# Performance work log

Measured on AMD Instinct MI355X. Metric: run time of the kernel, lower is better.

Reference implementation:

```python
import jax, jax.numpy as jnp
import numpy as np

D = 1024      # d_model
H = 16        # num_heads
HW = D // H   # head_width = 64
FF = 4 * D    # hidden_dim = 4096
BATCH = 2
T = 2048
EPS = 1e-5


def layer_norm(x, g, b):
    mu = jnp.mean(x, axis=-1, keepdims=True)
    var = jnp.mean(jnp.square(x - mu), axis=-1, keepdims=True)
    return (x - mu) * jax.lax.rsqrt(var + EPS) * g + b


def setup_inputs() -> dict:
    key = jax.random.key(0)
    ks = jax.random.split(key, 7)
    s = 0.02
    return {
        "x": jax.random.normal(ks[0], (BATCH, T, D), dtype=jnp.float32),
        "Wq": jax.random.normal(ks[1], (D, D), dtype=jnp.float32) * s,
        "Wk": jax.random.normal(ks[2], (D, D), dtype=jnp.float32) * s,
        "Wv": jax.random.normal(ks[3], (D, D), dtype=jnp.float32) * s,
        "W1": jax.random.normal(ks[4], (FF, D), dtype=jnp.float32) * s,
        "W2": jax.random.normal(ks[5], (D, FF), dtype=jnp.float32) * s,
        "g1": jnp.ones((D,), dtype=jnp.float32),
        "b1": jnp.zeros((D,), dtype=jnp.float32),
        "g2": jnp.ones((D,), dtype=jnp.float32),
        "b2": jnp.zeros((D,), dtype=jnp.float32),
    }


def reference(x, Wq, Wk, Wv, W1, W2, g1, b1, g2, b2):
    N, t, d = x.shape
    # norm1
    xn = layer_norm(x, g1, b1)

    # --- MHSA with ALiBi + causal mask (math mirrors torch module) ---
    def heads(y):  # (N,t,D) -> (N,H,t,HW)
        return y.reshape(N, t, H, HW).transpose(0, 2, 1, 3)

    q = heads(xn @ Wq.T)
    k = heads(xn @ Wk.T)
    v = heads(xn @ Wv.T)

    scores = jnp.einsum("nhqd,nhkd->nhqk", q, k) / np.sqrt(HW).astype(np.float32)

    pos = jnp.arange(t)
    rel = (pos[None, :] - pos[:, None]).astype(x.dtype)           # [t,t], rel[i,j]=j-i
    slopes = (2.0 ** (-(jnp.arange(1, H + 1)) * (8.0 / H))).astype(x.dtype)  # [H]
    alibi = slopes[:, None, None] * rel                            # [H,t,t]
    causal = jnp.where(pos[None, :] > pos[:, None],
                       jnp.array(-jnp.inf, x.dtype),
                       jnp.array(0.0, x.dtype))                    # [t,t]

    att = jax.nn.softmax(scores + alibi[None] + causal[None, None], axis=-1)
    o = jnp.einsum("nhqk,nhkd->nhqd", att, v)
    o = o.transpose(0, 2, 1, 3).reshape(N, t, d)

    att_out = xn + o

    # --- MLP: Linear -> SiLU -> Linear ---
    h = layer_norm(att_out, g2, b2)
    m = jax.nn.silu(h @ W1.T) @ W2.T
    return att_out + m
```

## Files before the change

### kernel.cpp

```cpp
#include <hip/hip_runtime.h>

#define DMODEL 1024
#define NHEAD  16
#define HWID   64
#define FFDIM  4096
#define NBATCH 2
#define SEQT   2048
#define NTOK   4096
#define QKLD   3072

using bf8    = __attribute__((ext_vector_type(8))) short;
using f32x4  = __attribute__((ext_vector_type(4))) float;
using f32x16 = __attribute__((ext_vector_type(16))) float;

__device__ inline short to_bf16(float f) {
  unsigned u = __float_as_uint(f);
  return (short)((u + 0x7fffu + ((u >> 16) & 1u)) >> 16);
}
__device__ inline float from_bf16(short s) {
  return __uint_as_float(((unsigned)(unsigned short)s) << 16);
}
__device__ inline float exp2_fast(float x) {
  float r;
  asm("v_exp_f32 %0, %1" : "=v"(r) : "v"(x));
  return r;
}
__device__ inline unsigned cvt_pk_bf16(float lo, float hi) {
  unsigned r;
  asm("v_cvt_pk_bf16_f32 %0, %1, %2" : "=v"(r) : "v"(lo), "v"(hi));
  return r;
}
__device__ inline void lds_load16(const void* g, void* l) {
  __builtin_amdgcn_global_load_lds(
      (const __attribute__((address_space(1))) void*)g,
      (__attribute__((address_space(3))) void*)l, 16, 0, 0);
}

__global__ __launch_bounds__(256)
void cvt_all(const float* __restrict__ Wq, const float* __restrict__ Wk,
             const float* __restrict__ Wv, const float* __restrict__ W1,
             const float* __restrict__ W2, short* __restrict__ wqkv,
             short* __restrict__ w1b, short* __restrict__ w2b) {
  int i = blockIdx.x * 256 + threadIdx.x;
  const float* src;
  short* dst;
  if (i < 1048576)      { src = W1; dst = w1b; }
  else if (i < 2097152) { src = W2; dst = w2b;            i -= 1048576; }
  else if (i < 2359296) { src = Wq; dst = wqkv;           i -= 2097152; }
  else if (i < 2621440) { src = Wk; dst = wqkv + 1048576; i -= 2359296; }
  else                  { src = Wv; dst = wqkv + 2097152; i -= 2621440; }
  float4 v = ((const float4*)src)[i];
  short4 o;
  o.x = to_bf16(v.x); o.y = to_bf16(v.y);
  o.z = to_bf16(v.z); o.w = to_bf16(v.w);
  ((short4*)dst)[i] = o;
}

__global__ __launch_bounds__(256)
void ln_kernel(const float* __restrict__ x, const float* __restrict__ g,
               const float* __restrict__ b, short* __restrict__ out) {
  const int row = blockIdx.x;
  const int t = threadIdx.x;
  const float4 v = ((const float4*)(x + (long)row * DMODEL))[t];
  float s  = v.x + v.y + v.z + v.w;
  float s2 = v.x * v.x + v.y * v.y + v.z * v.z + v.w * v.w;
#pragma unroll
  for (int m = 1; m < 64; m <<= 1) {
    s  += __shfl_xor(s, m);
    s2 += __shfl_xor(s2, m);
  }
  __shared__ float red[8];
  if ((t & 63) == 0) { red[t >> 6] = s; red[4 + (t >> 6)] = s2; }
  __syncthreads();
  s  = red[0] + red[1] + red[2] + red[3];
  s2 = red[4] + red[5] + red[6] + red[7];
  const float mu = s * (1.f / DMODEL);
  const float rs = rsqrtf(s2 * (1.f / DMODEL) - mu * mu + 1e-5f);
  const float4 gv = ((const float4*)g)[t];
  const float4 bv = ((const float4*)b)[t];
  short4 o;
  o.x = to_bf16((v.x - mu) * rs * gv.x + bv.x);
  o.y = to_bf16((v.y - mu) * rs * gv.y + bv.y);
  o.z = to_bf16((v.z - mu) * rs * gv.z + bv.z);
  o.w = to_bf16((v.w - mu) * rs * gv.w + bv.w);
  ((short4*)(out + (long)row * DMODEL))[t] = o;
}

template <int EPI>
__global__ __launch_bounds__(512, 2)
void gemm8r(const short* __restrict__ A, const short* __restrict__ Bw,
            void* __restrict__ Cout, int N, int lda, int ldb, int Kslice,
            long zstride) {
  __shared__ short lds[4][16384];
  const int tid = threadIdx.x;
  const int wid = tid >> 6, lane = tid & 63;
  const int l15 = lane & 15, l4 = lane >> 4;
  const int wm = wid >> 2, wn = wid & 3;

  const int gx = gridDim.x, nwg = gx * gridDim.y;
  const int wg = blockIdx.y * gx + blockIdx.x;
  const int sw = (wg & 7) * (nwg >> 3) + (wg >> 3);
  const int sx = gx >> 2;
  const int st = sw >> 4, w16 = sw & 15;
  const long bm = (long)((st / sx) * 4 + (w16 >> 2)) * 256;
  const long bn = (long)((st % sx) * 4 + (w16 & 3)) * 256;
  const long kofs = (long)blockIdx.z * Kslice;

  long aoff[2], boff[2];
  int  doff[2];
#pragma unroll
  for (int l = 0; l < 2; ++l) {
    const int gid = l * 512 + tid;
    const int row = gid >> 2;
    const int sg = (gid & 3) ^ ((row >> 1) & 3);
    aoff[l] = (bm + row) * (long)lda + kofs + sg * 8;
    boff[l] = (bn + row) * (long)ldb + kofs + sg * 8;
    doff[l] = gid * 16;
  }
  int offA[8], offB[4];
#pragma unroll
  for (int m = 0; m < 8; ++m) {
    const int row = wm * 128 + m * 16 + l15;
    offA[m] = row * 64 + ((l4 ^ ((row >> 1) & 3)) << 4);
  }
#pragma unroll
  for (int n = 0; n < 4; ++n) {
    const int row = wn * 64 + n * 16 + l15;
    offB[n] = row * 64 + ((l4 ^ ((row >> 1) & 3)) << 4);
  }

  const int NT = Kslice >> 5;
  f32x4 acc[8][4] = {};
  bf8 fa0[8], fb0[4], fa1[8], fb1[4];

#pragma unroll
  for (int tt = 0; tt < 3; ++tt) {
    char* db = (char*)&lds[tt][0];
#pragma unroll
    for (int l = 0; l < 2; ++l) {
      lds_load16(A  + aoff[l] + tt * 32, db + doff[l]);
      lds_load16(Bw + boff[l] + tt * 32, db + 16384 + doff[l]);
    }
  }
  asm volatile("s_waitcnt vmcnt(8)" ::: "memory");
  __builtin_amdgcn_s_barrier();
  asm volatile("" ::: "memory");
  {
    const char* sb = (const char*)&lds[0][0];
#pragma unroll
    for (int m = 0; m < 8; ++m) fa0[m] = *(const bf8*)(sb + offA[m]);
#pragma unroll
    for (int n = 0; n < 4; ++n) fb0[n] = *(const bf8*)(sb + 16384 + offB[n]);
  }

  auto step = [&](int t, bf8 (&ca)[8], bf8 (&cb)[4],
                  bf8 (&na)[8], bf8 (&nb)[4]) {
    if (t + 3 < NT) asm volatile("s_waitcnt vmcnt(4)" ::: "memory");
    else            asm volatile("s_waitcnt vmcnt(0)" ::: "memory");
    __builtin_amdgcn_s_barrier();
    asm volatile("" ::: "memory");
    if (t + 3 < NT) {
      char* db = (char*)&lds[(t + 3) & 3][0];
      const long ks = (long)(t + 3) * 32;
#pragma unroll
      for (int l = 0; l < 2; ++l) {
        lds_load16(A  + aoff[l] + ks, db + doff[l]);
        lds_load16(Bw + boff[l] + ks, db + 16384 + doff[l]);
      }
    }
    if (t + 1 < NT) {
      const char* sb = (const char*)&lds[(t + 1) & 3][0];
#pragma unroll
      for (int m = 0; m < 8; ++m) na[m] = *(const bf8*)(sb + offA[m]);
#pragma unroll
      for (int n = 0; n < 4; ++n) nb[n] = *(const bf8*)(sb + 16384 + offB[n]);
    }
    __builtin_amdgcn_sched_barrier(0);
    __builtin_amdgcn_s_setprio(1);
#pragma unroll
    for (int m = 0; m < 8; ++m)
#pragma unroll
      for (int n = 0; n < 4; ++n)
        acc[m][n] = __builtin_amdgcn_mfma_f32_16x16x32_bf16(ca[m], cb[n], acc[m][n], 0, 0, 0);
    __builtin_amdgcn_s_setprio(0);
  };

  for (int t = 0; t < NT; t += 2) {
    step(t,     fa0, fb0, fa1, fb1);
    step(t + 1, fa1, fb1, fa0, fb0);
  }

  float* Cp = (float*)Cout + (EPI == 2 ? (long)blockIdx.z * zstride : 0);
#pragma unroll
  for (int m = 0; m < 8; ++m)
#pragma unroll
    for (int n = 0; n < 4; ++n) {
      const long col = bn + wn * 64 + n * 16 + l15;
#pragma unroll
      for (int r = 0; r < 4; ++r) {
        const long row = bm + wm * 128 + m * 16 + l4 * 4 + r;
        float v = acc[m][n][r];
        if (EPI == 0) {
          ((short*)Cout)[row * N + col] = to_bf16(v);
        } else if (EPI == 1) {
          ((short*)Cout)[row * N + col] = to_bf16(v / (1.f + __expf(-v)));
        } else {
          Cp[row * N + col] = v;
        }
      }
    }
}

__global__ __launch_bounds__(256)
void pack_kv(const short* __restrict__ qkv, short* __restrict__ Kp,
             short* __restrict__ Vp) {
  __shared__ short tile[64][72];
  const int bx = blockIdx.x, bh = blockIdx.y;
  const int b = bh >> 4, h = bh & 15;
  const int t = threadIdx.x;
  if (bx < 64) {
    const int g = bx;
    const int row = t >> 3, cc = t & 7, c = cc >> 1, hi = cc & 1;
    const bf8 v = *(const bf8*)&qkv[(long)(b * SEQT + g * 32 + row) * QKLD +
                                    1024 + h * HWID + c * 16 + hi * 8];
    *(bf8*)&Kp[(((long)bh * 256 + g * 4 + c) * 64 + hi * 32 + row) * 8] = v;
  } else {
    const int tc = bx - 64;
    {
      const int r = t >> 2, c = (t & 3) * 16;
      const long src = (long)(b * SEQT + tc * 64 + r) * QKLD + 2048 + h * HWID + c;
      *(bf8*)&tile[r][c]     = *(const bf8*)&qkv[src];
      *(bf8*)&tile[r][c + 8] = *(const bf8*)&qkv[src + 8];
    }
    __syncthreads();
    const int dg = t >> 7, ch = (t >> 5) & 3, row = t & 31;
#pragma unroll
    for (int hi = 0; hi < 2; ++hi) {
      short o[8];
#pragma unroll
      for (int j = 0; j < 8; ++j) o[j] = tile[ch * 16 + hi * 8 + j][dg * 32 + row];
      *(bf8*)&Vp[(((long)bh * 256 + dg * 128 + tc * 4 + ch) * 64 + hi * 32 + row) * 8] =
          *(bf8*)o;
    }
  }
}

__global__ __launch_bounds__(64, 2)
void attn_kernel(const short* __restrict__ qkv, const short* __restrict__ Kp,
                 const short* __restrict__ Vp, const short* __restrict__ xn,
                 float* __restrict__ att) {
  const int L = blockIdx.x;
  const int bh = (L & 7) * 4 + ((L >> 3) & 3);
  const int qtile = 63 - (L >> 5);
  const int b = bh >> 4, h = bh & 15;
  const int q0 = qtile * 32;
  const int lane = threadIdx.x;
  const int l31 = lane & 31, hi = lane >> 5;
  const long tokbase = (long)b * SEQT;

  bf8 qf[4];
  {
    const short* qrow = qkv + (tokbase + q0 + l31) * QKLD + h * HWID + hi * 8;
#pragma unroll
    for (int c = 0; c < 4; ++c) qf[c] = *(const bf8*)(qrow + c * 16);
  }

  const float slope2 = exp2f(-0.5f * (float)(h + 1)) * 1.44269504f;
  const float sc2 = 0.125f * 1.44269504f;
  float arr[16];
#pragma unroll
  for (int r = 0; r < 16; ++r) arr[r] = slope2 * (float)((r & 3) + 8 * (r >> 2));
  const float hofs = slope2 * 4.f * (float)hi;
  const float qabs = (float)(q0 + l31);

  float m2 = -1e30f, lsum = 0.f;
  f32x16 acc0 = {}, acc1 = {};
  const int ktm = q0 >> 6;
  const bf8* kfb = (const bf8*)Kp + (long)bh * 16384 + lane;
  const bf8* vfb = (const bf8*)Vp + (long)bh * 16384 + lane;

  bf8 kc[8], kn[8], vc[8];
#pragma unroll
  for (int c = 0; c < 4; ++c) {
    kc[c]     = kfb[c * 64];
    kc[4 + c] = kfb[256 + c * 64];
  }

#pragma unroll 2
  for (int kt = 0; kt <= ktm; ++kt) {
    const int k0 = kt * 64;
    const long vb = (long)kt * 256;
#pragma unroll
    for (int ch = 0; ch < 4; ++ch) {
      vc[ch]     = vfb[vb + ch * 64];
      vc[4 + ch] = vfb[8192 + vb + ch * 64];
    }
    const long nb = (long)(kt < ktm ? kt + 1 : kt) * 512;
#pragma unroll
    for (int c = 0; c < 4; ++c) {
      kn[c]     = kfb[nb + c * 64];
      kn[4 + c] = kfb[nb + 256 + c * 64];
    }
    f32x16 s0 = {}, s1 = {};
#pragma unroll
    for (int c = 0; c < 4; ++c) {
      s0 = __builtin_amdgcn_mfma_f32_32x32x16_bf16(kc[c], qf[c], s0, 0, 0, 0);
      s1 = __builtin_amdgcn_mfma_f32_32x32x16_bf16(kc[4 + c], qf[c], s1, 0, 0, 0);
    }
    const float base = slope2 * ((float)k0 - qabs) + hofs;
    float s[32];
#pragma unroll
    for (int r = 0; r < 16; ++r) {
      s[r]      = fmaf(s0[r], sc2, base + arr[r]);
      s[16 + r] = fmaf(s1[r], sc2, base + arr[r] + slope2 * 32.f);
    }
    if (kt == ktm) {
      const int qi = q0 + l31;
#pragma unroll
      for (int r = 0; r < 16; ++r) {
        const int krel = (r & 3) + 8 * (r >> 2) + 4 * hi;
        if (k0 + krel > qi)      s[r]      = -1e30f;
        if (k0 + 32 + krel > qi) s[16 + r] = -1e30f;
      }
    }
    float ma = s[0], mb = s[1], mc = s[2], md = s[3];
#pragma unroll
    for (int i = 4; i < 32; i += 4) {
      ma = fmaxf(ma, s[i]); mb = fmaxf(mb, s[i + 1]);
      mc = fmaxf(mc, s[i + 2]); md = fmaxf(md, s[i + 3]);
    }
    float pm = fmaxf(fmaxf(ma, mb), fmaxf(mc, md));
    pm = fmaxf(pm, __shfl_xor(pm, 32));
    if (!__all(pm - m2 <= 11.0f)) {
      const float nm = fmaxf(m2, pm);
      const float alpha = exp2_fast(m2 - nm);
      m2 = nm;
      lsum *= alpha;
      acc0 *= alpha;
      acc1 *= alpha;
    }
    float p[32];
#pragma unroll
    for (int i = 0; i < 32; ++i) p[i] = exp2_fast(s[i] - m2);
    float sa = p[0], sb = p[1], sc = p[2], sd = p[3];
#pragma unroll
    for (int i = 4; i < 32; i += 4) {
      sa += p[i]; sb += p[i + 1]; sc += p[i + 2]; sd += p[i + 3];
    }
    float rs = (sa + sb) + (sc + sd);
    rs += __shfl_xor(rs, 32);
    lsum += rs;
    unsigned cpk[16];
#pragma unroll
    for (int g = 0; g < 8; ++g) {
      cpk[g]     = cvt_pk_bf16(p[2 * g], p[2 * g + 1]);
      cpk[8 + g] = cvt_pk_bf16(p[16 + 2 * g], p[16 + 2 * g + 1]);
    }
    bf8 pb[4];
#pragma unroll
    for (int ch = 0; ch < 4; ++ch) {
      const int cb = (ch >> 1) * 8 + (ch & 1) * 4;
      unsigned u0 = cpk[cb + 0], u2 = cpk[cb + 2];
      unsigned u1 = cpk[cb + 1], u3 = cpk[cb + 3];
      asm("v_permlane32_swap_b32 %0, %1" : "+v"(u0), "+v"(u2));
      asm("v_permlane32_swap_b32 %0, %1" : "+v"(u1), "+v"(u3));
      union { unsigned u[4]; bf8 v; } f;
      f.u[0] = u0; f.u[1] = u1; f.u[2] = u2; f.u[3] = u3;
      pb[ch] = f.v;
    }
#pragma unroll
    for (int ch = 0; ch < 4; ++ch) {
      acc0 = __builtin_amdgcn_mfma_f32_32x32x16_bf16(vc[ch], pb[ch], acc0, 0, 0, 0);
      acc1 = __builtin_amdgcn_mfma_f32_32x32x16_bf16(vc[4 + ch], pb[ch], acc1, 0, 0, 0);
    }
#pragma unroll
    for (int i = 0; i < 8; ++i) kc[i] = kn[i];
  }

  __shared__ float Os[32 * 68];
  const float rl = 1.f / lsum;
#pragma unroll
  for (int r = 0; r < 16; ++r) {
    const int d0 = (r & 3) + 8 * (r >> 2) + 4 * hi;
    Os[l31 * 68 + d0]      = acc0[r] * rl;
    Os[l31 * 68 + 32 + d0] = acc1[r] * rl;
  }
  __syncthreads();
#pragma unroll
  for (int it = 0; it < 8; ++it) {
    const int idx = it * 64 + lane;
    const int row = idx >> 4, c4 = idx & 15;
    const float4 ov = *(const float4*)&Os[row * 68 + c4 * 4];
    const long gbase = (tokbase + q0 + row) * DMODEL + h * HWID + c4 * 4;
    const short4 xv = *(const short4*)&xn[gbase];
    float4 o;
    o.x = ov.x + from_bf16(xv.x);
    o.y = ov.y + from_bf16(xv.y);
    o.z = ov.z + from_bf16(xv.z);
    o.w = ov.w + from_bf16(xv.w);
    *(float4*)&att[gbase] = o;
  }
}

__global__ __launch_bounds__(256)
void combine_kernel(const float* __restrict__ p, float* __restrict__ dout, int n4) {
  int i = blockIdx.x * 256 + threadIdx.x;
  if (i < n4) {
    float4 a  = ((const float4*)dout)[i];
    float4 b0 = ((const float4*)(p))[i];
    float4 b1 = ((const float4*)(p + 4194304))[i];
    float4 b2 = ((const float4*)(p + 8388608))[i];
    float4 b3 = ((const float4*)(p + 12582912))[i];
    a.x += (b0.x + b1.x) + (b2.x + b3.x);
    a.y += (b0.y + b1.y) + (b2.y + b3.y);
    a.z += (b0.z + b1.z) + (b2.z + b3.z);
    a.w += (b0.w + b1.w) + (b2.w + b3.w);
    ((float4*)dout)[i] = a;
  }
}

extern "C" void kernel_launch(void* const* d_in, const int* in_sizes, int n_in,
                              void* d_out, int out_size, void* d_ws, size_t ws_size,
                              hipStream_t stream) {
  (void)in_sizes; (void)n_in; (void)out_size; (void)ws_size;
  const float* x  = (const float*)d_in[0];
  const float* Wq = (const float*)d_in[1];
  const float* Wk = (const float*)d_in[2];
  const float* Wv = (const float*)d_in[3];
  const float* W1 = (const float*)d_in[4];
  const float* W2 = (const float*)d_in[5];
  const float* g1 = (const float*)d_in[6];
  const float* b1 = (const float*)d_in[7];
  const float* g2 = (const float*)d_in[8];
  const float* b2 = (const float*)d_in[9];

  char* ws = (char*)d_ws;
  const size_t MB = 1024 * 1024;
  short* wqkv_b = (short*)(ws + 0);
  short* w1_b   = (short*)(ws + 6  * MB);
  short* w2_b   = (short*)(ws + 14 * MB);
  short* xn     = (short*)(ws + 22 * MB);
  short* qkv    = (short*)(ws + 30 * MB);
  short* m1     = (short*)(ws + 22 * MB);
  short* Kp     = (short*)(ws + 54 * MB);
  short* Vp     = (short*)(ws + 62 * MB);
  short* hb     = (short*)(ws + 70 * MB);
  float* parts  = (float*)(ws + 54 * MB);
  float* att    = (float*)d_out;

  cvt_all<<<11264, 256, 0, stream>>>(Wq, Wk, Wv, W1, W2, wqkv_b, w1_b, w2_b);

  ln_kernel<<<NTOK, 256, 0, stream>>>(x, g1, b1, xn);

  gemm8r<0><<<dim3(12, 16), 512, 0, stream>>>(xn, wqkv_b, qkv, QKLD, DMODEL, DMODEL,
                                              DMODEL, 0);
  pack_kv<<<dim3(96, 32), 256, 0, stream>>>(qkv, Kp, Vp);

  attn_kernel<<<2048, 64, 0, stream>>>(qkv, Kp, Vp, xn, att);

  ln_kernel<<<NTOK, 256, 0, stream>>>(att, g2, b2, hb);

  gemm8r<1><<<dim3(16, 16), 512, 0, stream>>>(hb, w1_b, m1, FFDIM, DMODEL, DMODEL,
                                              DMODEL, 0);
  gemm8r<2><<<dim3(4, 16, 4), 512, 0, stream>>>(m1, w2_b, parts, DMODEL, FFDIM, FFDIM,
                                                1024, (long)NTOK * DMODEL);
  combine_kernel<<<4096, 256, 0, stream>>>(parts, (float*)d_out, 1048576);
}
```

Measured before the change: 204.8 us.

## Restructure GEMM into 64-wide K tiles with half-staged double-buffered LDS phases

New measurement: 209.0 us. 1.02x slower.

```diff
diff --git a/kernel.cpp b/kernel.cpp
--- a/kernel.cpp
+++ b/kernel.cpp
@@ -88,10 +88,10 @@
 
 template <int EPI>
 __global__ __launch_bounds__(512, 2)
-void gemm8r(const short* __restrict__ A, const short* __restrict__ Bw,
-            void* __restrict__ Cout, int N, int lda, int ldb, int Kslice,
-            long zstride) {
-  __shared__ short lds[4][16384];
+void gemm256(const short* __restrict__ A, const short* __restrict__ Bw,
+             void* __restrict__ Cout, int N, int lda, int ldb, int Kslice,
+             long zstride) {
+  __shared__ short lds[2][2][16384];
   const int tid = threadIdx.x;
   const int wid = tid >> 6, lane = tid & 63;
   const int l15 = lane & 15, l4 = lane >> 4;
@@ -105,101 +105,119 @@
   const long bm = (long)((st / sx) * 4 + (w16 >> 2)) * 256;
   const long bn = (long)((st % sx) * 4 + (w16 & 3)) * 256;
   const long kofs = (long)blockIdx.z * Kslice;
-
-  long aoff[2], boff[2];
-  int  doff[2];
+  const int NT = Kslice >> 6;
+
+  long arow[2], brow[2];
+  int  sgel[2], dofs[2];
 #pragma unroll
   for (int l = 0; l < 2; ++l) {
-    const int gid = l * 512 + tid;
-    const int row = gid >> 2;
-    const int sg = (gid & 3) ^ ((row >> 1) & 3);
-    aoff[l] = (bm + row) * (long)lda + kofs + sg * 8;
-    boff[l] = (bn + row) * (long)ldb + kofs + sg * 8;
-    doff[l] = gid * 16;
-  }
-  int offA[8], offB[4];
-#pragma unroll
-  for (int m = 0; m < 8; ++m) {
-    const int row = wm * 128 + m * 16 + l15;
-    offA[m] = row * 64 + ((l4 ^ ((row >> 1) & 3)) << 4);
-  }
-#pragma unroll
-  for (int n = 0; n < 4; ++n) {
-    const int row = wn * 64 + n * 16 + l15;
-    offB[n] = row * 64 + ((l4 ^ ((row >> 1) & 3)) << 4);
-  }
-
-  const int NT = Kslice >> 5;
+    const int g = l * 512 + tid;
+    const int row = g >> 2;
+    sgel[l] = ((g & 3) ^ (row & 3)) * 8;
+    dofs[l] = g * 16;
+    arow[l] = (bm + row) * (long)lda + kofs;
+    brow[l] = (bn + row) * (long)ldb + kofs;
+  }
+  auto stage_half = [&](int h) {
+    if (h >= (NT << 2)) return;
+    const int th = h >> 2, hi = h & 3, buf = th & 1;
+    const int ks = hi >> 1, isA = hi & 1;
+    char* db = (char*)&lds[buf][isA ? 0 : 1][0] + ks * 16384;
+    const long kb = (long)th * 64 + ks * 32;
+#pragma unroll
+    for (int l = 0; l < 2; ++l) {
+      const short* src = (isA ? A + arow[l] : Bw + brow[l]) + kb + sgel[l];
+      lds_load16(src, db + dofs[l]);
+    }
+  };
+
+  const int xsw = (l4 ^ (l15 & 3)) << 4;
+  const int aofs = (wm * 128 + l15) * 64 + xsw;
+  const int bofs = (wn * 64 + l15) * 64 + xsw;
+
   f32x4 acc[8][4] = {};
-  bf8 fa0[8], fb0[4], fa1[8], fb1[4];
-
-#pragma unroll
-  for (int tt = 0; tt < 3; ++tt) {
-    char* db = (char*)&lds[tt][0];
-#pragma unroll
-    for (int l = 0; l < 2; ++l) {
-      lds_load16(A  + aoff[l] + tt * 32, db + doff[l]);
-      lds_load16(Bw + boff[l] + tt * 32, db + 16384 + doff[l]);
-    }
-  }
-  asm volatile("s_waitcnt vmcnt(8)" ::: "memory");
+  bf8 fa[4], fa2[4], fb[4];
+
+#define PH_MID                                             \
+  __builtin_amdgcn_s_barrier();                            \
+  asm volatile("s_waitcnt lgkmcnt(0)" ::: "memory");       \
+  __builtin_amdgcn_sched_barrier(0);                       \
+  __builtin_amdgcn_s_setprio(1);
+#define PH_END                                             \
+  __builtin_amdgcn_s_setprio(0);                           \
+  __builtin_amdgcn_s_barrier();                            \
+  asm volatile("" ::: "memory");
+
+#pragma unroll
+  for (int h = 0; h < 7; ++h) stage_half(h);
+  asm volatile("s_waitcnt vmcnt(6)" ::: "memory");
   __builtin_amdgcn_s_barrier();
   asm volatile("" ::: "memory");
-  {
-    const char* sb = (const char*)&lds[0][0];
-#pragma unroll
-    for (int m = 0; m < 8; ++m) fa0[m] = *(const bf8*)(sb + offA[m]);
-#pragma unroll
-    for (int n = 0; n < 4; ++n) fb0[n] = *(const bf8*)(sb + 16384 + offB[n]);
-  }
-
-  auto step = [&](int t, bf8 (&ca)[8], bf8 (&cb)[4],
-                  bf8 (&na)[8], bf8 (&nb)[4]) {
-    if (t + 3 < NT) asm volatile("s_waitcnt vmcnt(4)" ::: "memory");
-    else            asm volatile("s_waitcnt vmcnt(0)" ::: "memory");
-    __builtin_amdgcn_s_barrier();
-    asm volatile("" ::: "memory");
-    if (t + 3 < NT) {
-      char* db = (char*)&lds[(t + 3) & 3][0];
-      const long ks = (long)(t + 3) * 32;
-#pragma unroll
-      for (int l = 0; l < 2; ++l) {
-        lds_load16(A  + aoff[l] + ks, db + doff[l]);
-        lds_load16(Bw + boff[l] + ks, db + 16384 + doff[l]);
-      }
-    }
-    if (t + 1 < NT) {
-      const char* sb = (const char*)&lds[(t + 1) & 3][0];
-#pragma unroll
-      for (int m = 0; m < 8; ++m) na[m] = *(const bf8*)(sb + offA[m]);
-#pragma unroll
-      for (int n = 0; n < 4; ++n) nb[n] = *(const bf8*)(sb + 16384 + offB[n]);
-    }
-    __builtin_amdgcn_sched_barrier(0);
-    __builtin_amdgcn_s_setprio(1);
-#pragma unroll
-    for (int m = 0; m < 8; ++m)
+
+  for (int u = 0; u < NT; ++u) {
+    const int buf = u & 1;
+    const char* pa = (const char*)&lds[buf][0][0];
+    const char* pb = (const char*)&lds[buf][1][0];
+#pragma unroll
+    for (int m = 0; m < 4; ++m) fa[m] = *(const bf8*)(pa + aofs + m * 1024);
+#pragma unroll
+    for (int n = 0; n < 4; ++n) fb[n] = *(const bf8*)(pb + bofs + n * 1024);
+    stage_half(4 * u + 7);
+    PH_MID
+#pragma unroll
+    for (int m = 0; m < 4; ++m)
 #pragma unroll
       for (int n = 0; n < 4; ++n)
-        acc[m][n] = __builtin_amdgcn_mfma_f32_16x16x32_bf16(ca[m], cb[n], acc[m][n], 0, 0, 0);
-    __builtin_amdgcn_s_setprio(0);
-  };
-
-  for (int t = 0; t < NT; t += 2) {
-    step(t,     fa0, fb0, fa1, fb1);
-    step(t + 1, fa1, fb1, fa0, fb0);
-  }
+        acc[m][n] = __builtin_amdgcn_mfma_f32_16x16x32_bf16(fa[m], fb[n], acc[m][n], 0, 0, 0);
+    PH_END
+#pragma unroll
+    for (int m = 0; m < 4; ++m) fa2[m] = *(const bf8*)(pa + aofs + (4 + m) * 1024);
+    stage_half(4 * u + 8);
+    PH_MID
+#pragma unroll
+    for (int m = 0; m < 4; ++m)
+#pragma unroll
+      for (int n = 0; n < 4; ++n)
+        acc[4 + m][n] = __builtin_amdgcn_mfma_f32_16x16x32_bf16(fa2[m], fb[n], acc[4 + m][n], 0, 0, 0);
+    PH_END
+#pragma unroll
+    for (int m = 0; m < 4; ++m) fa[m] = *(const bf8*)(pa + 16384 + aofs + m * 1024);
+#pragma unroll
+    for (int n = 0; n < 4; ++n) fb[n] = *(const bf8*)(pb + 16384 + bofs + n * 1024);
+    stage_half(4 * u + 9);
+    PH_MID
+#pragma unroll
+    for (int m = 0; m < 4; ++m)
+#pragma unroll
+      for (int n = 0; n < 4; ++n)
+        acc[m][n] = __builtin_amdgcn_mfma_f32_16x16x32_bf16(fa[m], fb[n], acc[m][n], 0, 0, 0);
+    PH_END
+#pragma unroll
+    for (int m = 0; m < 4; ++m) fa2[m] = *(const bf8*)(pa + 16384 + aofs + (4 + m) * 1024);
+    stage_half(4 * u + 10);
+    if (u <= NT - 3)      asm volatile("s_waitcnt vmcnt(6)" ::: "memory");
+    else if (u == NT - 2) asm volatile("s_waitcnt vmcnt(0)" ::: "memory");
+    PH_MID
+#pragma unroll
+    for (int m = 0; m < 4; ++m)
+#pragma unroll
+      for (int n = 0; n < 4; ++n)
+        acc[4 + m][n] = __builtin_amdgcn_mfma_f32_16x16x32_bf16(fa2[m], fb[n], acc[4 + m][n], 0, 0, 0);
+    PH_END
+  }
+#undef PH_MID
+#undef PH_END
 
   float* Cp = (float*)Cout + (EPI == 2 ? (long)blockIdx.z * zstride : 0);
 #pragma unroll
-  for (int m = 0; m < 8; ++m)
+  for (int mg = 0; mg < 8; ++mg)
 #pragma unroll
     for (int n = 0; n < 4; ++n) {
       const long col = bn + wn * 64 + n * 16 + l15;
 #pragma unroll
       for (int r = 0; r < 4; ++r) {
-        const long row = bm + wm * 128 + m * 16 + l4 * 4 + r;
-        float v = acc[m][n][r];
+        const long row = bm + wm * 128 + mg * 16 + l4 * 4 + r;
+        float v = acc[mg][n][r];
         if (EPI == 0) {
           ((short*)Cout)[row * N + col] = to_bf16(v);
         } else if (EPI == 1) {
@@ -251,7 +269,8 @@
                  float* __restrict__ att) {
   const int L = blockIdx.x;
   const int bh = (L & 7) * 4 + ((L >> 3) & 3);
-  const int qtile = 63 - (L >> 5);
+  const int u = L >> 5;
+  const int qtile = (u < 32) ? (63 - u) : (u - 32);
   const int b = bh >> 4, h = bh & 15;
   const int q0 = qtile * 32;
   const int lane = threadIdx.x;
@@ -452,17 +471,17 @@
 
   ln_kernel<<<NTOK, 256, 0, stream>>>(x, g1, b1, xn);
 
-  gemm8r<0><<<dim3(12, 16), 512, 0, stream>>>(xn, wqkv_b, qkv, QKLD, DMODEL, DMODEL,
-                                              DMODEL, 0);
+  gemm256<0><<<dim3(12, 16), 512, 0, stream>>>(xn, wqkv_b, qkv, QKLD, DMODEL, DMODEL,
+                                               DMODEL, 0);
   pack_kv<<<dim3(96, 32), 256, 0, stream>>>(qkv, Kp, Vp);
 
   attn_kernel<<<2048, 64, 0, stream>>>(qkv, Kp, Vp, xn, att);
 
   ln_kernel<<<NTOK, 256, 0, stream>>>(att, g2, b2, hb);
 
-  gemm8r<1><<<dim3(16, 16), 512, 0, stream>>>(hb, w1_b, m1, FFDIM, DMODEL, DMODEL,
-                                              DMODEL, 0);
-  gemm8r<2><<<dim3(4, 16, 4), 512, 0, stream>>>(m1, w2_b, parts, DMODEL, FFDIM, FFDIM,
-                                                1024, (long)NTOK * DMODEL);
+  gemm256<1><<<dim3(16, 16), 512, 0, stream>>>(hb, w1_b, m1, FFDIM, DMODEL, DMODEL,
+                                               DMODEL, 0);
+  gemm256<2><<<dim3(4, 16, 4), 512, 0, stream>>>(m1, w2_b, parts, DMODEL, FFDIM, FFDIM,
+                                                 1024, (long)NTOK * DMODEL);
   combine_kernel<<<4096, 256, 0, stream>>>(parts, (float*)d_out, 1048576);
 }
```
